# Performance work log

Measured on AMD Instinct MI355X. Metric: run time of the kernel, lower is better.

Reference implementation:

```python
import jax, jax.numpy as jnp
import numpy as np

NUM_BLOCKS = 16  # 4x4 grid of 2x2 blocks over the 8x8 matrix
E_BLK, H_BLK = 4, 2
E_CROSS, H_CROSS = 64, 8
VOCAB = 32000
LN_EPS = 1e-5


def _mha(x, Wqkv, bqkv, Wo, bo, nheads):
    """torch nn.MultiheadAttention (batch_first, self-attn, eval mode).
    Returns (out [B,T,E], attn weights averaged over heads [B,T,T])."""
    B, T, E = x.shape
    Dh = E // nheads
    qkv = x @ Wqkv.T + bqkv                      # [B,T,3E]
    q, k, v = jnp.split(qkv, 3, axis=-1)
    sp = lambda t: t.reshape(B, T, nheads, Dh).transpose(0, 2, 1, 3)  # [B,H,T,Dh]
    q, k, v = sp(q), sp(k), sp(v)
    scale = 1.0 / float(np.sqrt(Dh))
    scores = jnp.einsum('bhqd,bhkd->bhqk', q, k) * scale
    attn = jax.nn.softmax(scores, axis=-1)
    out = jnp.einsum('bhqk,bhkd->bhqd', attn, v).transpose(0, 2, 1, 3).reshape(B, T, E)
    return out @ Wo.T + bo, attn.mean(axis=1)


def _layernorm(x, g, b):
    mu = x.mean(-1, keepdims=True)
    var = x.var(-1, keepdims=True)
    return (x - mu) * jax.lax.rsqrt(var + LN_EPS) * g + b


def _to_blocks(M):
    # [B,T,8,8] -> [B,T,16,4]; block i = (row_blk*4+col_blk), 2x2 flattened row-major
    B, T = M.shape[:2]
    return jnp.transpose(M.reshape(B, T, 4, 2, 4, 2), (0, 1, 2, 4, 3, 5)).reshape(B, T, 16, 4)


def _from_blocks(x):
    # [B,T,16,4] -> [B,T,8,8]
    B, T = x.shape[:2]
    return jnp.transpose(x.reshape(B, T, 4, 4, 2, 2), (0, 1, 2, 4, 3, 5)).reshape(B, T, 8, 8)


def setup_inputs() -> dict:
    key = jax.random.key(0)
    ks = jax.random.split(key, 24)
    B, T = 4, 1024
    s = 0.05
    return {
        'M': jax.random.normal(ks[0], (B, T, 8, 8), jnp.float32),
        'token_ids': jax.random.randint(ks[1], (B, T), 0, VOCAB, jnp.int64),
        # 16 per-block MHA param sets (stacked)
        'Wqkv_blk': jax.random.normal(ks[2], (NUM_BLOCKS, 3 * E_BLK, E_BLK), jnp.float32) * s,
        'bqkv_blk': jnp.zeros((NUM_BLOCKS, 3 * E_BLK), jnp.float32),
        'Wo_blk': jax.random.normal(ks[3], (NUM_BLOCKS, E_BLK, E_BLK), jnp.float32) * s,
        'bo_blk': jnp.zeros((NUM_BLOCKS, E_BLK), jnp.float32),
        # cross-block MHA
        'Wqkv_c': jax.random.normal(ks[4], (3 * E_CROSS, E_CROSS), jnp.float32) * s,
        'bqkv_c': jnp.zeros((3 * E_CROSS,), jnp.float32),
        'Wo_c': jax.random.normal(ks[5], (E_CROSS, E_CROSS), jnp.float32) * s,
        'bo_c': jnp.zeros((E_CROSS,), jnp.float32),
        # FFN 64 -> 256 -> 64
        'W1': jax.random.normal(ks[6], (256, 64), jnp.float32) * s,
        'b1': jnp.zeros((256,), jnp.float32),
        'W2': jax.random.normal(ks[7], (64, 256), jnp.float32) * s,
        'b2': jnp.zeros((64,), jnp.float32),
        # LayerNorms
        'g1': jnp.ones((64,), jnp.float32), 'be1': jnp.zeros((64,), jnp.float32),
        'g2': jnp.ones((64,), jnp.float32), 'be2': jnp.zeros((64,), jnp.float32),
        # DynamicBlockSensitivity params
        'sens_emb': jax.random.normal(ks[8], (VOCAB, NUM_BLOCKS), jnp.float32) * s,
        'sens_alpha': jax.random.normal(ks[9], (NUM_BLOCKS,), jnp.float32) * s,
    }


def reference(M, token_ids, Wqkv_blk, bqkv_blk, Wo_blk, bo_blk,
              Wqkv_c, bqkv_c, Wo_c, bo_c, W1, b1, W2, b2,
              g1, be1, g2, be2, sens_emb, sens_alpha):
    B, T = M.shape[:2]
    blocks = _to_blocks(M)                                # [B,T,16,4]
    x_blk = jnp.moveaxis(blocks, 2, 0)                    # [16,B,T,4]
    blk_out, _ = jax.vmap(lambda x, W, b, Wo, bo: _mha(x, W, b, Wo, bo, H_BLK))(
        x_blk, Wqkv_blk, bqkv_blk, Wo_blk, bo_blk)        # [16,B,T,4]
    all_blocks = jnp.moveaxis(blk_out, 0, 2).reshape(B, T, 64)
    cross_out, attn_w = _mha(all_blocks, Wqkv_c, bqkv_c, Wo_c, bo_c, H_CROSS)
    all_blocks = _layernorm(all_blocks + cross_out, g1, be1)
    ffn = jax.nn.gelu(all_blocks @ W1.T + b1, approximate=False) @ W2.T + b2
    all_blocks = _layernorm(all_blocks + ffn, g2, be2)
    # Dynamic block sensitivity: token embedding + attention-received modulation
    attn_recv = attn_w.mean(axis=1)                       # [B,T] attention each token receives
    sens = jax.nn.sigmoid(sens_emb[token_ids] + attn_recv[..., None] * sens_alpha)  # [B,T,16]
    new_blocks = blocks + (all_blocks.reshape(B, T, 16, 4) - blocks) * sens[..., None]
    return _from_blocks(new_blocks)
```

## Files before the change

kernel.cpp:

```cpp
#include <hip/hip_runtime.h>
#include <hip/hip_bf16.h>
#include <math.h>

#define BB 4
#define TT 1024
#define BT 4096

#define OFF_BLOCKS 0
#define OFF_QKVB   262144
#define OFF_RECVP  262144
#define OFF_ALLB   1048576
#define OFF_QKVC   1310720
#define OFF_LC     2097152
#define OFF_ACCC   2129920
#define OFF_LN1    2396160
#define OFF_PARAMS 2658304
#define WS_FLOATS  2708624

#define P_W1T    0
#define P_W2T    16384
#define P_WQCT   32768
#define P_WOCT   45056
#define P_WOBLK  49152
#define P_BOBLK  49408
#define P_BQC    49472
#define P_BOC    49664
#define P_G1     49728
#define P_BE1    49792
#define P_B1     49856
#define P_B2     50112
#define P_G2     50176
#define P_BE2    50240
#define P_SAL    50304
#define P_TOTAL  50320

__device__ inline float rcpf(float x) { return __builtin_amdgcn_rcpf(x); }

typedef _Float16 h2 __attribute__((ext_vector_type(2)));
typedef __fp16   fh2 __attribute__((ext_vector_type(2)));

__device__ inline uint pkh(float a, float b) {
#if __has_builtin(__builtin_amdgcn_cvt_pkrtz)
  fh2 r = __builtin_amdgcn_cvt_pkrtz(a, b);
  return __builtin_bit_cast(uint, r);
#else
  h2 r = { (_Float16)a, (_Float16)b };
  return __builtin_bit_cast(uint, r);
#endif
}
__device__ inline h2 toh2(uint u) { return __builtin_bit_cast(h2, u); }

__device__ inline float dot2h(h2 a, h2 b, float c) {
#if __has_builtin(__builtin_amdgcn_fdot2)
  return __builtin_amdgcn_fdot2(a, b, c, false);
#else
  return c + (float)a.x * (float)b.x + (float)a.y * (float)b.y;
#endif
}

__device__ inline bool detect_bf16(const void* M) {
  const unsigned short* h = (const unsigned short*)M;
  unsigned short v = h[threadIdx.x & 63];
  int e = (v >> 7) & 0xff;
  unsigned long long m = __ballot((e >= 90) && (e <= 141));
  return __popcll(m) >= 58;
}

template <bool ISBF>
__device__ inline float ldf(const void* p, int i) {
  if (ISBF) return __bfloat162float(((const __hip_bfloat16*)p)[i]);
  else      return ((const float*)p)[i];
}

template <bool ISBF>
__global__ void __launch_bounds__(256) k_prep2(
    const void* __restrict__ M,
    const void* __restrict__ Wqkv_blk,
    const void* __restrict__ bqkv_blk,
    const void* __restrict__ W1, const void* __restrict__ W2,
    const void* __restrict__ Wqkv_c, const void* __restrict__ Wo_c,
    const void* __restrict__ Wo_blk, const void* __restrict__ bo_blk,
    const void* __restrict__ bqkv_c, const void* __restrict__ bo_c,
    const void* __restrict__ g1, const void* __restrict__ be1,
    const void* __restrict__ b1, const void* __restrict__ b2,
    const void* __restrict__ g2, const void* __restrict__ be2,
    const void* __restrict__ sens_al,
    float* __restrict__ blocks, float* __restrict__ qkv_blk,
    float* __restrict__ params) {
  if (detect_bf16(M) != ISBF) return;
  if (blockIdx.x < 256) {
    int g = blockIdx.x * 256 + threadIdx.x;
    int i = g >> 12, bt = g & 4095;
    int rb = i >> 2, cb = i & 3;
    float x[4];
    #pragma unroll
    for (int r = 0; r < 2; ++r)
      #pragma unroll
      for (int c = 0; c < 2; ++c)
        x[r*2+c] = ldf<ISBF>(M, bt*64 + (rb*2+r)*8 + cb*2 + c);
    float* bo = blocks + bt*64 + i*4;
    #pragma unroll
    for (int j = 0; j < 4; ++j) bo[j] = x[j];
    float* o = qkv_blk + (i*BT + bt) * 12;
    #pragma unroll
    for (int c = 0; c < 12; ++c) {
      float a = ldf<ISBF>(bqkv_blk, i*12 + c);
      #pragma unroll
      for (int j = 0; j < 4; ++j) a += ldf<ISBF>(Wqkv_blk, i*48 + c*4 + j) * x[j];
      o[c] = a;
    }
  } else {
    for (int o = (blockIdx.x - 256)*256 + threadIdx.x; o < P_TOTAL; o += 16*256) {
      float v;
      if      (o < 16384) { int j = o >> 8, h2_ = o & 255; v = ldf<ISBF>(W1, h2_*64 + j); }
      else if (o < 32768) { int q = o - 16384; int k = q >> 6, j = q & 63; v = ldf<ISBF>(W2, j*256 + k); }
      else if (o < 45056) { int q = o - 32768; int j = q / 192, c = q % 192; v = ldf<ISBF>(Wqkv_c, c*64 + j); }
      else if (o < 49152) { int q = o - 45056; int m = q >> 6, j = q & 63; v = ldf<ISBF>(Wo_c, j*64 + m); }
      else if (o < 49408) v = ldf<ISBF>(Wo_blk, o - 49152);
      else if (o < 49472) v = ldf<ISBF>(bo_blk, o - 49408);
      else if (o < 49664) v = ldf<ISBF>(bqkv_c, o - 49472);
      else if (o < 49728) v = ldf<ISBF>(bo_c,   o - 49664);
      else if (o < 49792) v = ldf<ISBF>(g1,     o - 49728);
      else if (o < 49856) v = ldf<ISBF>(be1,    o - 49792);
      else if (o < 50112) v = ldf<ISBF>(b1,     o - 49856);
      else if (o < 50176) v = ldf<ISBF>(b2,     o - 50112);
      else if (o < 50240) v = ldf<ISBF>(g2,     o - 50176);
      else if (o < 50304) v = ldf<ISBF>(be2,    o - 50240);
      else                v = ldf<ISBF>(sens_al, o - 50304);
      params[o] = v;
    }
  }
}

__global__ void __launch_bounds__(512) k_blk2(
    const float* __restrict__ qkv_blk,
    const float* __restrict__ params,
    float* __restrict__ all_blocks) {
  __shared__ __align__(16) uint lds[14464];
  float* qf  = (float*)lds;
  uint*  kvu = lds + 4096;
  float* red = (float*)(lds + 8192);
  int bid = blockIdx.x;
  int qt = bid & 7, b = (bid >> 3) & 3, i = bid >> 5;
  int tid = threadIdx.x;
  int wv = __builtin_amdgcn_readfirstlane(tid) >> 6;
  int ql = tid & 63;
  const float* slab = qkv_blk + (size_t)(i*BT + b*TT) * 12;
  #pragma unroll
  for (int rr = 0; rr < 2; ++rr) {
    int r = tid + rr*512;
    const float4* rp = (const float4*)(slab + (size_t)r*12);
    float4 x0 = rp[0], x1 = rp[1], x2 = rp[2];
    *(float4*)(qf + r*4) = x0;
    *(uint4*)(kvu + r*4) = make_uint4(pkh(x1.x,x1.y), pkh(x1.z,x1.w),
                                      pkh(x2.x,x2.y), pkh(x2.z,x2.w));
  }
  __syncthreads();
  int qa = qt*128 + ql, qb = qa + 64;
  const float S2 = 0.70710678f;
  float4 qav = *(const float4*)(qf + qa*4);
  float4 qbv = *(const float4*)(qf + qb*4);
  uint qa01 = pkh(qav.x*S2, qav.y*S2), qa23 = pkh(qav.z*S2, qav.w*S2);
  uint qb01 = pkh(qbv.x*S2, qbv.y*S2), qb23 = pkh(qbv.z*S2, qbv.w*S2);
  float la0=0.f, la1=0.f, aa00=0.f, aa01=0.f, aa10=0.f, aa11=0.f;
  float lb0=0.f, lb1=0.f, ab00=0.f, ab01=0.f, ab10=0.f, ab11=0.f;
  int kbeg = wv*128;
  #pragma unroll 4
  for (int k = kbeg; k < kbeg + 128; ++k) {
    uint4 kk = *(const uint4*)(kvu + k*4);
    h2 k01 = toh2(kk.x), k23 = toh2(kk.y);
    h2 v01 = toh2(kk.z), v23 = toh2(kk.w);
    float pa0 = __expf(dot2h(toh2(qa01), k01, 0.f));
    float pa1 = __expf(dot2h(toh2(qa23), k23, 0.f));
    float pb0 = __expf(dot2h(toh2(qb01), k01, 0.f));
    float pb1 = __expf(dot2h(toh2(qb23), k23, 0.f));
    la0 += pa0; aa00 += pa0*(float)v01.x; aa01 += pa0*(float)v01.y;
    la1 += pa1; aa10 += pa1*(float)v23.x; aa11 += pa1*(float)v23.y;
    lb0 += pb0; ab00 += pb0*(float)v01.x; ab01 += pb0*(float)v01.y;
    lb1 += pb1; ab10 += pb1*(float)v23.x; ab11 += pb1*(float)v23.y;
  }
  float* ra = red + ql*49 + wv*6;
  ra[0]=la0; ra[1]=la1; ra[2]=aa00; ra[3]=aa01; ra[4]=aa10; ra[5]=aa11;
  float* rb = red + (ql+64)*49 + wv*6;
  rb[0]=lb0; rb[1]=lb1; rb[2]=ab00; rb[3]=ab01; rb[4]=ab10; rb[5]=ab11;
  __syncthreads();
  if (tid < 128) {
    float s[6] = {0.f,0.f,0.f,0.f,0.f,0.f};
    #pragma unroll
    for (int w = 0; w < 8; ++w) {
      const float* p = red + tid*49 + w*6;
      #pragma unroll
      for (int c = 0; c < 6; ++c) s[c] += p[c];
    }
    float r0 = rcpf(s[0]), r1 = rcpf(s[1]);
    float o[4] = { s[2]*r0, s[3]*r0, s[4]*r1, s[5]*r1 };
    int q2 = qt*128 + tid;
    const float* pWo = params + P_WOBLK + i*16;
    float* outp = all_blocks + (size_t)(b*TT + q2)*64 + i*4;
    #pragma unroll
    for (int j = 0; j < 4; ++j) {
      float a = params[P_BOBLK + i*4 + j];
      #pragma unroll
      for (int m2 = 0; m2 < 4; ++m2) a += pWo[j*4 + m2] * o[m2];
      outp[j] = a;
    }
  }
}

__global__ void __launch_bounds__(256) k_qkv_c2(
    const float* __restrict__ all_blocks,
    const float* __restrict__ params,
    float* __restrict__ qkv_c) {
  __shared__ float w[12288];
  __shared__ float xs[256];
  int tid = threadIdx.x;
  int t0 = blockIdx.x * 4;
  {
    const float4* src = (const float4*)(params + P_WQCT);
    float4* dst = (float4*)w;
    #pragma unroll
    for (int i = tid; i < 3072; i += 256) dst[i] = src[i];
  }
  xs[tid] = all_blocks[t0*64 + tid];
  __syncthreads();
  int tt = tid >> 6, lane = tid & 63;
  int t = t0 + tt;
  const float* x = xs + tt*64;
  float a0 = params[P_BQC + lane];
  float a1 = params[P_BQC + 64 + lane];
  float a2 = params[P_BQC + 128 + lane];
  #pragma unroll 8
  for (int j = 0; j < 64; ++j) {
    const float* r = w + j*192;
    float xj = x[j];
    a0 += r[lane]       * xj;
    a1 += r[64 + lane]  * xj;
    a2 += r[128 + lane] * xj;
  }
  float* o = qkv_c + (size_t)t*192;
  o[lane] = a0; o[64 + lane] = a1; o[128 + lane] = a2;
}

__global__ void __launch_bounds__(1024) k_cross9(
    const float* __restrict__ qkv_c,
    float* __restrict__ acc_c,
    float* __restrict__ recv_part) {
  __shared__ __align__(16) uint lds[23680];
  uint*  Ku  = lds;
  uint*  Vu  = lds + 4096;
  float* red = (float*)(lds + 4096);
  uint*  qb_ = lds + 22656;
  int bid = blockIdx.x;
  int qt = bid & 7, h = (bid >> 3) & 7, b = bid >> 6;
  int tid = threadIdx.x;
  int wv = __builtin_amdgcn_readfirstlane(tid) >> 6;
  int ql = tid & 63;
  int h8 = h*8;
  const float* base = qkv_c + (size_t)b*TT*192;
  {
    int r = tid;
    const float4* kp = (const float4*)(base + (size_t)r*192 + 64 + h8);
    const float4* vp = (const float4*)(base + (size_t)r*192 + 128 + h8);
    float4 k0 = kp[0], k1 = kp[1], v0 = vp[0], v1 = vp[1];
    *(uint4*)(Ku + r*4) = make_uint4(pkh(k0.x,k0.y), pkh(k0.z,k0.w),
                                     pkh(k1.x,k1.y), pkh(k1.z,k1.w));
    *(uint4*)(Vu + r*4) = make_uint4(pkh(v0.x,v0.y), pkh(v0.z,v0.w),
                                     pkh(v1.x,v1.y), pkh(v1.z,v1.w));
  }
  int qa = qt*128 + ql, qbq = qa + 64;
  const float SC = 0.35355339f;
  uint qa01,qa23,qa45,qa67, qb01,qb23,qb45,qb67;
  {
    const float4* pa = (const float4*)(base + (size_t)qa*192 + h8);
    const float4* pb = (const float4*)(base + (size_t)qbq*192 + h8);
    float4 a0 = pa[0], a1 = pa[1], b0 = pb[0], b1 = pb[1];
    qa01 = pkh(a0.x*SC, a0.y*SC); qa23 = pkh(a0.z*SC, a0.w*SC);
    qa45 = pkh(a1.x*SC, a1.y*SC); qa67 = pkh(a1.z*SC, a1.w*SC);
    qb01 = pkh(b0.x*SC, b0.y*SC); qb23 = pkh(b0.z*SC, b0.w*SC);
    qb45 = pkh(b1.x*SC, b1.y*SC); qb67 = pkh(b1.z*SC, b1.w*SC);
  }
  __syncthreads();
  float la = 0.f, lb = 0.f, aca[8], acb[8];
  #pragma unroll
  for (int c = 0; c < 8; ++c) { aca[c] = 0.f; acb[c] = 0.f; }
  int kbeg = wv*64;
  #pragma unroll 4
  for (int k = kbeg; k < kbeg + 64; ++k) {
    uint4 kk = *(const uint4*)(Ku + k*4);
    uint4 vv = *(const uint4*)(Vu + k*4);
    h2 k01 = toh2(kk.x), k23 = toh2(kk.y), k45 = toh2(kk.z), k67 = toh2(kk.w);
    float sa = dot2h(toh2(qa01),k01, dot2h(toh2(qa23),k23,
               dot2h(toh2(qa45),k45, dot2h(toh2(qa67),k67, 0.f))));
    float sb = dot2h(toh2(qb01),k01, dot2h(toh2(qb23),k23,
               dot2h(toh2(qb45),k45, dot2h(toh2(qb67),k67, 0.f))));
    float pa = __expf(sa);
    float pb = __expf(sb);
    la += pa; lb += pb;
    h2 v01 = toh2(vv.x), v23 = toh2(vv.y), v45 = toh2(vv.z), v67 = toh2(vv.w);
    aca[0] += pa*(float)v01.x; aca[1] += pa*(float)v01.y;
    aca[2] += pa*(float)v23.x; aca[3] += pa*(float)v23.y;
    aca[4] += pa*(float)v45.x; aca[5] += pa*(float)v45.y;
    aca[6] += pa*(float)v67.x; aca[7] += pa*(float)v67.y;
    acb[0] += pb*(float)v01.x; acb[1] += pb*(float)v01.y;
    acb[2] += pb*(float)v23.x; acb[3] += pb*(float)v23.y;
    acb[4] += pb*(float)v45.x; acb[5] += pb*(float)v45.y;
    acb[6] += pb*(float)v67.x; acb[7] += pb*(float)v67.y;
  }
  __syncthreads();
  {
    float* ra = red + ql*145 + wv*9;
    ra[0] = la;
    #pragma unroll
    for (int c = 0; c < 8; ++c) ra[1+c] = aca[c];
    float* rb = red + (ql+64)*145 + wv*9;
    rb[0] = lb;
    #pragma unroll
    for (int c = 0; c < 8; ++c) rb[1+c] = acb[c];
    if (wv == 0) {
      *(uint4*)(qb_ + ql*8)      = make_uint4(qa01, qa23, qa45, qa67);
      *(uint4*)(qb_ + (ql+64)*8) = make_uint4(qb01, qb23, qb45, qb67);
    }
  }
  __syncthreads();
  if (tid < 128) {
    float ls = 0.f, as[8];
    #pragma unroll
    for (int c = 0; c < 8; ++c) as[c] = 0.f;
    #pragma unroll
    for (int w = 0; w < 16; ++w) {
      const float* p = red + tid*145 + w*9;
      ls += p[0];
      #pragma unroll
      for (int c = 0; c < 8; ++c) as[c] += p[1+c];
    }
    float invl = rcpf(ls);
    int q2 = qt*128 + tid;
    int idx = (b*8 + h)*TT + q2;
    float4 o0 = { as[0]*invl, as[1]*invl, as[2]*invl, as[3]*invl };
    float4 o1 = { as[4]*invl, as[5]*invl, as[6]*invl, as[7]*invl };
    float4* op = (float4*)(acc_c + (size_t)idx*8);
    op[0] = o0; op[1] = o1;
    ((float*)(qb_ + tid*8))[4] = -__log2f(ls);
  }
  __syncthreads();
  {
    int qh = wv >> 3, g = wv & 7;
    int p = g*64 + ql;
    uint4 ka = *(const uint4*)(Ku + p*4);
    uint4 kb = *(const uint4*)(Ku + (p+512)*4);
    h2 A0 = toh2(ka.x), A1 = toh2(ka.y), A2 = toh2(ka.z), A3 = toh2(ka.w);
    h2 B0 = toh2(kb.x), B1 = toh2(kb.y), B2 = toh2(kb.z), B3 = toh2(kb.w);
    float r0 = 0.f, r1 = 0.f;
    const uint* qrow = qb_ + qh*64*8;
    const float L2E = 1.44269504f;
    #pragma unroll 4
    for (int qq = 0; qq < 64; ++qq) {
      uint4 q4 = *(const uint4*)(qrow + qq*8);
      float mq = __uint_as_float(qrow[qq*8 + 4]);
      h2 Q0 = toh2(q4.x), Q1 = toh2(q4.y), Q2 = toh2(q4.z), Q3 = toh2(q4.w);
      float s0 = dot2h(Q0,A0, dot2h(Q1,A1, dot2h(Q2,A2, dot2h(Q3,A3, 0.f))));
      float s1 = dot2h(Q0,B0, dot2h(Q1,B1, dot2h(Q2,B2, dot2h(Q3,B3, 0.f))));
      r0 += exp2f(fmaf(s0, L2E, mq));
      r1 += exp2f(fmaf(s1, L2E, mq));
    }
    int src = h*16 + qt*2 + qh;
    recv_part[((size_t)(b*1024 + p      ))*128 + src] = r0;
    recv_part[((size_t)(b*1024 + p + 512))*128 + src] = r1;
  }
}

__global__ void __launch_bounds__(256) k_fin(
    const float* __restrict__ all_blocks,
    const float* __restrict__ acc_c,
    const float* __restrict__ params,
    float* __restrict__ ln1) {
  __shared__ float pvs[4*64];
  int tt = threadIdx.x >> 6, j = threadIdx.x & 63;
  int t = blockIdx.x*4 + tt;
  int b = t >> 10, tl = t & 1023;
  int h = j >> 3;
  int idx = (b*8 + h)*TT + tl;
  pvs[tt*64 + j] = acc_c[idx*8 + (j & 7)];
  __syncthreads();
  float a = params[P_BOC + j];
  const float* WoT = params + P_WOCT;
  const float* p = pvs + tt*64;
  #pragma unroll 8
  for (int m = 0; m < 64; ++m) a += WoT[m*64 + j] * p[m];
  float x = all_blocks[t*64 + j] + a;
  float s = x, s2 = x*x;
  #pragma unroll
  for (int off = 32; off; off >>= 1) { s += __shfl_xor(s, off); s2 += __shfl_xor(s2, off); }
  float mu  = s  * (1.f/64.f);
  float var = s2 * (1.f/64.f) - mu*mu;
  float y = (x - mu) * rsqrtf(var + 1e-5f) * params[P_G1 + j] + params[P_BE1 + j];
  ln1[t*64 + j] = y;
}

template <bool ISBF>
__global__ void __launch_bounds__(512) k_ffn_out2(
    const void* __restrict__ M,
    const float* __restrict__ ln1,
    const float* __restrict__ params,
    const float* __restrict__ blocks,
    const int* __restrict__ tok32,
    const float* __restrict__ recv_part,
    const void* __restrict__ sens_emb,
    void* __restrict__ out) {
  if (detect_bf16(M) != ISBF) return;
  __shared__ float w[16384];
  __shared__ float ld2[512];
  __shared__ float hbuf[2048];
  int tid = threadIdx.x;
  int t0 = blockIdx.x * 8;
  int wv = tid >> 6, lane = tid & 63;
  float recv;
  {
    int t = t0 + wv, b = t >> 10, k = t & 1023;
    const float* rp = recv_part + ((size_t)(b*1024 + k))*128;
    float s = rp[lane] + rp[lane + 64];
    #pragma unroll
    for (int off = 32; off; off >>= 1) s += __shfl_xor(s, off);
    recv = s * (1.f/8192.f);
  }
  ld2[lane*8 + wv] = ln1[(t0 + wv)*64 + lane];
  {
    const float4* src = (const float4*)(params + P_W1T);
    float4* dst = (float4*)w;
    #pragma unroll
    for (int i = tid; i < 4096; i += 512) dst[i] = src[i];
  }
  __syncthreads();
  {
    int g = tid >> 8, u = tid & 255;
    float a0, a1, a2, a3;
    a0 = a1 = a2 = a3 = params[P_B1 + u];
    #pragma unroll 8
    for (int j = 0; j < 64; ++j) {
      float wj = w[j*256 + u];
      float4 xj = *(const float4*)(ld2 + j*8 + g*4);
      a0 += wj*xj.x; a1 += wj*xj.y; a2 += wj*xj.z; a3 += wj*xj.w;
    }
    float av[4] = {a0, a1, a2, a3};
    #pragma unroll
    for (int t2 = 0; t2 < 4; ++t2) {
      float v = av[t2];
      float u2 = 1.5957691f*v + 0.07135481f*v*v*v;
      hbuf[(g*4 + t2)*256 + u] = v * rcpf(1.f + __expf(-u2));
    }
  }
  __syncthreads();
  {
    const float4* src = (const float4*)(params + P_W2T);
    float4* dst = (float4*)w;
    #pragma unroll
    for (int i = tid; i < 4096; i += 512) dst[i] = src[i];
  }
  __syncthreads();
  int j = lane;
  int t = t0 + wv, b = t >> 10;
  float y = params[P_B2 + j];
  const float* hb = hbuf + wv*256;
  #pragma unroll 8
  for (int k = 0; k < 256; ++k) y += w[k*64 + j] * hb[k];
  float z = ld2[j*8 + wv] + y;
  float s = z, s2 = z*z;
  #pragma unroll
  for (int off = 32; off; off >>= 1) { s += __shfl_xor(s, off); s2 += __shfl_xor(s2, off); }
  float mu  = s  * (1.f/64.f);
  float var = s2 * (1.f/64.f) - mu*mu;
  float y2 = (z - mu) * rsqrtf(var + 1e-5f) * params[P_G2 + j] + params[P_BE2 + j];
  bool is64 = ((tok32[1] | tok32[3] | tok32[5] | tok32[7]) == 0);
  int tok = is64 ? tok32[t*2] : tok32[t];
  int i = j >> 2, e = j & 3;
  float sv = ldf<ISBF>(sens_emb, tok*16 + i) + recv * params[P_SAL + i];
  float sg = rcpf(1.f + __expf(-sv));
  float blk = blocks[t*64 + j];
  float nb = blk + (y2 - blk) * sg;
  int rb = i >> 2, cb = i & 3, r = e >> 1, c = e & 1;
  int oidx = t*64 + (rb*2 + r)*8 + cb*2 + c;
  if (ISBF) ((__hip_bfloat16*)out)[oidx] = __float2bfloat16(nb);
  else      ((float*)out)[oidx] = nb;
}

extern "C" void kernel_launch(void* const* d_in, const int* in_sizes, int n_in,
                              void* d_out, int out_size, void* d_ws, size_t ws_size,
                              hipStream_t stream) {
  const void* M        = d_in[0];
  const int*  tok      = (const int*)d_in[1];
  const void* Wqkv_blk = d_in[2];
  const void* bqkv_blk = d_in[3];
  const void* Wo_blk   = d_in[4];
  const void* bo_blk   = d_in[5];
  const void* Wqkv_c   = d_in[6];
  const void* bqkv_c   = d_in[7];
  const void* Wo_c     = d_in[8];
  const void* bo_c     = d_in[9];
  const void* W1       = d_in[10];
  const void* b1       = d_in[11];
  const void* W2       = d_in[12];
  const void* b2       = d_in[13];
  const void* g1       = d_in[14];
  const void* be1      = d_in[15];
  const void* g2i      = d_in[16];
  const void* be2      = d_in[17];
  const void* sens_emb = d_in[18];
  const void* sens_al  = d_in[19];

  float* ws = (float*)d_ws;
  float* blocks    = ws + OFF_BLOCKS;
  float* qkv_blk   = ws + OFF_QKVB;
  float* recv_part = ws + OFF_RECVP;
  float* all_blk   = ws + OFF_ALLB;
  float* qkv_c     = ws + OFF_QKVC;
  float* acc_c     = ws + OFF_ACCC;
  float* ln1       = ws + OFF_LN1;
  float* params    = ws + OFF_PARAMS;

  k_prep2<true ><<<272, 256, 0, stream>>>(M, Wqkv_blk, bqkv_blk, W1, W2, Wqkv_c, Wo_c,
                                          Wo_blk, bo_blk, bqkv_c, bo_c, g1, be1, b1, b2,
                                          g2i, be2, sens_al, blocks, qkv_blk, params);
  k_prep2<false><<<272, 256, 0, stream>>>(M, Wqkv_blk, bqkv_blk, W1, W2, Wqkv_c, Wo_c,
                                          Wo_blk, bo_blk, bqkv_c, bo_c, g1, be1, b1, b2,
                                          g2i, be2, sens_al, blocks, qkv_blk, params);
  k_blk2<<<512, 512, 0, stream>>>(qkv_blk, params, all_blk);
  k_qkv_c2<<<1024, 256, 0, stream>>>(all_blk, params, qkv_c);
  k_cross9<<<256, 1024, 0, stream>>>(qkv_c, acc_c, recv_part);
  k_fin<<<1024, 256, 0, stream>>>(all_blk, acc_c, params, ln1);
  k_ffn_out2<true ><<<512, 512, 0, stream>>>(M, ln1, params, blocks, tok, recv_part,
                                             sens_emb, (void*)d_out);
  k_ffn_out2<false><<<512, 512, 0, stream>>>(M, ln1, params, blocks, tok, recv_part,
                                             sens_emb, (void*)d_out);
}
```

Baseline: 204.8 us.

## Merge dtype-dispatched launches, fold log2e into scales, restructure recv and FFN reductions

Replaces the paired bf16/fp32 template launches with single kernels that branch on detected dtype internally, removing two redundant launches. Folds log2(e) into the query scales so the attention loops use exp2f directly. Reorganises the cross-attention received-attention pass to combine partial sums in LDS, halving the recv_part width. Splits the FFN second matmul across waves with an LDS reduction so each wave covers a k-slice for all 8 tokens. Adds LDS traffic and extra barriers in exchange.

After: 217.8 us. 1.06x slower.

```diff
diff --git a/kernel.cpp b/kernel.cpp
--- a/kernel.cpp
+++ b/kernel.cpp
@@ -73,21 +73,13 @@
 }
 
 template <bool ISBF>
-__global__ void __launch_bounds__(256) k_prep2(
-    const void* __restrict__ M,
-    const void* __restrict__ Wqkv_blk,
-    const void* __restrict__ bqkv_blk,
-    const void* __restrict__ W1, const void* __restrict__ W2,
-    const void* __restrict__ Wqkv_c, const void* __restrict__ Wo_c,
-    const void* __restrict__ Wo_blk, const void* __restrict__ bo_blk,
-    const void* __restrict__ bqkv_c, const void* __restrict__ bo_c,
-    const void* __restrict__ g1, const void* __restrict__ be1,
-    const void* __restrict__ b1, const void* __restrict__ b2,
-    const void* __restrict__ g2, const void* __restrict__ be2,
-    const void* __restrict__ sens_al,
-    float* __restrict__ blocks, float* __restrict__ qkv_blk,
-    float* __restrict__ params) {
-  if (detect_bf16(M) != ISBF) return;
+__device__ void prep2_body(
+    const void* M, const void* Wqkv_blk, const void* bqkv_blk,
+    const void* W1, const void* W2, const void* Wqkv_c, const void* Wo_c,
+    const void* Wo_blk, const void* bo_blk, const void* bqkv_c, const void* bo_c,
+    const void* g1, const void* be1, const void* b1, const void* b2,
+    const void* g2, const void* be2, const void* sens_al,
+    float* blocks, float* qkv_blk, float* params) {
   if (blockIdx.x < 256) {
     int g = blockIdx.x * 256 + threadIdx.x;
     int i = g >> 12, bt = g & 4095;
@@ -130,6 +122,29 @@
       params[o] = v;
     }
   }
+}
+
+__global__ void __launch_bounds__(256) k_prep3(
+    const void* __restrict__ M, const void* __restrict__ Wqkv_blk,
+    const void* __restrict__ bqkv_blk,
+    const void* __restrict__ W1, const void* __restrict__ W2,
+    const void* __restrict__ Wqkv_c, const void* __restrict__ Wo_c,
+    const void* __restrict__ Wo_blk, const void* __restrict__ bo_blk,
+    const void* __restrict__ bqkv_c, const void* __restrict__ bo_c,
+    const void* __restrict__ g1, const void* __restrict__ be1,
+    const void* __restrict__ b1, const void* __restrict__ b2,
+    const void* __restrict__ g2, const void* __restrict__ be2,
+    const void* __restrict__ sens_al,
+    float* __restrict__ blocks, float* __restrict__ qkv_blk,
+    float* __restrict__ params) {
+  if (detect_bf16(M))
+    prep2_body<true >(M, Wqkv_blk, bqkv_blk, W1, W2, Wqkv_c, Wo_c, Wo_blk, bo_blk,
+                      bqkv_c, bo_c, g1, be1, b1, b2, g2, be2, sens_al,
+                      blocks, qkv_blk, params);
+  else
+    prep2_body<false>(M, Wqkv_blk, bqkv_blk, W1, W2, Wqkv_c, Wo_c, Wo_blk, bo_blk,
+                      bqkv_c, bo_c, g1, be1, b1, b2, g2, be2, sens_al,
+                      blocks, qkv_blk, params);
 }
 
 __global__ void __launch_bounds__(512) k_blk2(
@@ -157,11 +172,11 @@
   }
   __syncthreads();
   int qa = qt*128 + ql, qb = qa + 64;
-  const float S2 = 0.70710678f;
+  const float S2L = 0.70710678f * 1.44269504f;
   float4 qav = *(const float4*)(qf + qa*4);
   float4 qbv = *(const float4*)(qf + qb*4);
-  uint qa01 = pkh(qav.x*S2, qav.y*S2), qa23 = pkh(qav.z*S2, qav.w*S2);
-  uint qb01 = pkh(qbv.x*S2, qbv.y*S2), qb23 = pkh(qbv.z*S2, qbv.w*S2);
+  uint qa01 = pkh(qav.x*S2L, qav.y*S2L), qa23 = pkh(qav.z*S2L, qav.w*S2L);
+  uint qb01 = pkh(qbv.x*S2L, qbv.y*S2L), qb23 = pkh(qbv.z*S2L, qbv.w*S2L);
   float la0=0.f, la1=0.f, aa00=0.f, aa01=0.f, aa10=0.f, aa11=0.f;
   float lb0=0.f, lb1=0.f, ab00=0.f, ab01=0.f, ab10=0.f, ab11=0.f;
   int kbeg = wv*128;
@@ -170,10 +185,10 @@
     uint4 kk = *(const uint4*)(kvu + k*4);
     h2 k01 = toh2(kk.x), k23 = toh2(kk.y);
     h2 v01 = toh2(kk.z), v23 = toh2(kk.w);
-    float pa0 = __expf(dot2h(toh2(qa01), k01, 0.f));
-    float pa1 = __expf(dot2h(toh2(qa23), k23, 0.f));
-    float pb0 = __expf(dot2h(toh2(qb01), k01, 0.f));
-    float pb1 = __expf(dot2h(toh2(qb23), k23, 0.f));
+    float pa0 = exp2f(dot2h(toh2(qa01), k01, 0.f));
+    float pa1 = exp2f(dot2h(toh2(qa23), k23, 0.f));
+    float pb0 = exp2f(dot2h(toh2(qb01), k01, 0.f));
+    float pb1 = exp2f(dot2h(toh2(qb23), k23, 0.f));
     la0 += pa0; aa00 += pa0*(float)v01.x; aa01 += pa0*(float)v01.y;
     la1 += pa1; aa10 += pa1*(float)v23.x; aa11 += pa1*(float)v23.y;
     lb0 += pb0; ab00 += pb0*(float)v01.x; ab01 += pb0*(float)v01.y;
@@ -241,15 +256,16 @@
   o[lane] = a0; o[64 + lane] = a1; o[128 + lane] = a2;
 }
 
-__global__ void __launch_bounds__(1024) k_cross9(
+__global__ void __launch_bounds__(1024) k_cross10(
     const float* __restrict__ qkv_c,
     float* __restrict__ acc_c,
     float* __restrict__ recv_part) {
   __shared__ __align__(16) uint lds[23680];
-  uint*  Ku  = lds;
-  uint*  Vu  = lds + 4096;
-  float* red = (float*)(lds + 4096);
-  uint*  qb_ = lds + 22656;
+  uint*  Ku   = lds;
+  uint*  Vu   = lds + 4096;
+  float* red  = (float*)(lds + 4096);
+  float* rcmb = (float*)(lds + 4096);
+  uint*  qb_  = lds + 22656;
   int bid = blockIdx.x;
   int qt = bid & 7, h = (bid >> 3) & 7, b = bid >> 6;
   int tid = threadIdx.x;
@@ -268,16 +284,16 @@
                                      pkh(v1.x,v1.y), pkh(v1.z,v1.w));
   }
   int qa = qt*128 + ql, qbq = qa + 64;
-  const float SC = 0.35355339f;
+  const float SCL = 0.35355339f * 1.44269504f;
   uint qa01,qa23,qa45,qa67, qb01,qb23,qb45,qb67;
   {
     const float4* pa = (const float4*)(base + (size_t)qa*192 + h8);
     const float4* pb = (const float4*)(base + (size_t)qbq*192 + h8);
     float4 a0 = pa[0], a1 = pa[1], b0 = pb[0], b1 = pb[1];
-    qa01 = pkh(a0.x*SC, a0.y*SC); qa23 = pkh(a0.z*SC, a0.w*SC);
-    qa45 = pkh(a1.x*SC, a1.y*SC); qa67 = pkh(a1.z*SC, a1.w*SC);
-    qb01 = pkh(b0.x*SC, b0.y*SC); qb23 = pkh(b0.z*SC, b0.w*SC);
-    qb45 = pkh(b1.x*SC, b1.y*SC); qb67 = pkh(b1.z*SC, b1.w*SC);
+    qa01 = pkh(a0.x*SCL, a0.y*SCL); qa23 = pkh(a0.z*SCL, a0.w*SCL);
+    qa45 = pkh(a1.x*SCL, a1.y*SCL); qa67 = pkh(a1.z*SCL, a1.w*SCL);
+    qb01 = pkh(b0.x*SCL, b0.y*SCL); qb23 = pkh(b0.z*SCL, b0.w*SCL);
+    qb45 = pkh(b1.x*SCL, b1.y*SCL); qb67 = pkh(b1.z*SCL, b1.w*SCL);
   }
   __syncthreads();
   float la = 0.f, lb = 0.f, aca[8], acb[8];
@@ -289,12 +305,12 @@
     uint4 kk = *(const uint4*)(Ku + k*4);
     uint4 vv = *(const uint4*)(Vu + k*4);
     h2 k01 = toh2(kk.x), k23 = toh2(kk.y), k45 = toh2(kk.z), k67 = toh2(kk.w);
-    float sa = dot2h(toh2(qa01),k01, dot2h(toh2(qa23),k23,
-               dot2h(toh2(qa45),k45, dot2h(toh2(qa67),k67, 0.f))));
-    float sb = dot2h(toh2(qb01),k01, dot2h(toh2(qb23),k23,
-               dot2h(toh2(qb45),k45, dot2h(toh2(qb67),k67, 0.f))));
-    float pa = __expf(sa);
-    float pb = __expf(sb);
+    float sa = dot2h(toh2(qa01),k01, dot2h(toh2(qa23),k23, 0.f))
+             + dot2h(toh2(qa45),k45, dot2h(toh2(qa67),k67, 0.f));
+    float sb = dot2h(toh2(qb01),k01, dot2h(toh2(qb23),k23, 0.f))
+             + dot2h(toh2(qb45),k45, dot2h(toh2(qb67),k67, 0.f));
+    float pa = exp2f(sa);
+    float pb = exp2f(sb);
     la += pa; lb += pb;
     h2 v01 = toh2(vv.x), v23 = toh2(vv.y), v45 = toh2(vv.z), v67 = toh2(vv.w);
     aca[0] += pa*(float)v01.x; aca[1] += pa*(float)v01.y;
@@ -344,28 +360,43 @@
   }
   __syncthreads();
   {
-    int qh = wv >> 3, g = wv & 7;
+    int qq = wv >> 2, g = wv & 3;
     int p = g*64 + ql;
     uint4 ka = *(const uint4*)(Ku + p*4);
-    uint4 kb = *(const uint4*)(Ku + (p+512)*4);
-    h2 A0 = toh2(ka.x), A1 = toh2(ka.y), A2 = toh2(ka.z), A3 = toh2(ka.w);
-    h2 B0 = toh2(kb.x), B1 = toh2(kb.y), B2 = toh2(kb.z), B3 = toh2(kb.w);
-    float r0 = 0.f, r1 = 0.f;
-    const uint* qrow = qb_ + qh*64*8;
-    const float L2E = 1.44269504f;
+    uint4 kb = *(const uint4*)(Ku + (p+256)*4);
+    uint4 kc = *(const uint4*)(Ku + (p+512)*4);
+    uint4 kd = *(const uint4*)(Ku + (p+768)*4);
+    float r0 = 0.f, r1 = 0.f, r2 = 0.f, r3 = 0.f;
+    const uint* qrow = qb_ + qq*32*8;
     #pragma unroll 4
-    for (int qq = 0; qq < 64; ++qq) {
-      uint4 q4 = *(const uint4*)(qrow + qq*8);
-      float mq = __uint_as_float(qrow[qq*8 + 4]);
+    for (int q = 0; q < 32; ++q) {
+      uint4 q4 = *(const uint4*)(qrow + q*8);
+      float mq = __uint_as_float(qrow[q*8 + 4]);
       h2 Q0 = toh2(q4.x), Q1 = toh2(q4.y), Q2 = toh2(q4.z), Q3 = toh2(q4.w);
-      float s0 = dot2h(Q0,A0, dot2h(Q1,A1, dot2h(Q2,A2, dot2h(Q3,A3, 0.f))));
-      float s1 = dot2h(Q0,B0, dot2h(Q1,B1, dot2h(Q2,B2, dot2h(Q3,B3, 0.f))));
-      r0 += exp2f(fmaf(s0, L2E, mq));
-      r1 += exp2f(fmaf(s1, L2E, mq));
-    }
-    int src = h*16 + qt*2 + qh;
-    recv_part[((size_t)(b*1024 + p      ))*128 + src] = r0;
-    recv_part[((size_t)(b*1024 + p + 512))*128 + src] = r1;
+      float s0 = dot2h(Q0,toh2(ka.x), dot2h(Q1,toh2(ka.y), 0.f))
+               + dot2h(Q2,toh2(ka.z), dot2h(Q3,toh2(ka.w), 0.f));
+      float s1 = dot2h(Q0,toh2(kb.x), dot2h(Q1,toh2(kb.y), 0.f))
+               + dot2h(Q2,toh2(kb.z), dot2h(Q3,toh2(kb.w), 0.f));
+      float s2 = dot2h(Q0,toh2(kc.x), dot2h(Q1,toh2(kc.y), 0.f))
+               + dot2h(Q2,toh2(kc.z), dot2h(Q3,toh2(kc.w), 0.f));
+      float s3 = dot2h(Q0,toh2(kd.x), dot2h(Q1,toh2(kd.y), 0.f))
+               + dot2h(Q2,toh2(kd.z), dot2h(Q3,toh2(kd.w), 0.f));
+      r0 += exp2f(s0 + mq);
+      r1 += exp2f(s1 + mq);
+      r2 += exp2f(s2 + mq);
+      r3 += exp2f(s3 + mq);
+    }
+    rcmb[(p      )*4 + qq] = r0;
+    rcmb[(p + 256)*4 + qq] = r1;
+    rcmb[(p + 512)*4 + qq] = r2;
+    rcmb[(p + 768)*4 + qq] = r3;
+  }
+  __syncthreads();
+  {
+    int k = tid;
+    float4 v = *(const float4*)(rcmb + k*4);
+    int src = h*8 + qt;
+    recv_part[((size_t)(b*1024 + k))*64 + src] = v.x + v.y + v.z + v.w;
   }
 }
 
@@ -398,7 +429,104 @@
 }
 
 template <bool ISBF>
-__global__ void __launch_bounds__(512) k_ffn_out2(
+__device__ void ffn_body(
+    const float* ln1, const float* params, const float* blocks,
+    const int* tok32, const float* recv_part, const void* sens_emb, void* out,
+    float* w, float* ld2, float* hbuf) {
+  int tid = threadIdx.x;
+  int t0 = blockIdx.x * 8;
+  int wv = tid >> 6, lane = tid & 63;
+  float recv;
+  {
+    int t = t0 + wv, b = t >> 10, k = t & 1023;
+    const float* rp = recv_part + ((size_t)(b*1024 + k))*64;
+    float s = rp[lane];
+    #pragma unroll
+    for (int off = 32; off; off >>= 1) s += __shfl_xor(s, off);
+    recv = s * (1.f/8192.f);
+  }
+  ld2[lane*8 + wv] = ln1[(t0 + wv)*64 + lane];
+  {
+    const float4* src = (const float4*)(params + P_W1T);
+    float4* dst = (float4*)w;
+    #pragma unroll
+    for (int i = tid; i < 4096; i += 512) dst[i] = src[i];
+  }
+  __syncthreads();
+  {
+    int g = tid >> 8, u = tid & 255;
+    float a0, a1, a2, a3;
+    a0 = a1 = a2 = a3 = params[P_B1 + u];
+    #pragma unroll 8
+    for (int j = 0; j < 64; ++j) {
+      float wj = w[j*256 + u];
+      float4 xj = *(const float4*)(ld2 + j*8 + g*4);
+      a0 += wj*xj.x; a1 += wj*xj.y; a2 += wj*xj.z; a3 += wj*xj.w;
+    }
+    float av[4] = {a0, a1, a2, a3};
+    float4 hv;
+    #pragma unroll
+    for (int t2 = 0; t2 < 4; ++t2) {
+      float v = av[t2];
+      float u2 = 1.5957691f*v + 0.07135481f*v*v*v;
+      ((float*)&hv)[t2] = v * rcpf(1.f + __expf(-u2));
+    }
+    *(float4*)(hbuf + u*8 + g*4) = hv;
+  }
+  __syncthreads();
+  {
+    const float4* src = (const float4*)(params + P_W2T);
+    float4* dst = (float4*)w;
+    #pragma unroll
+    for (int i = tid; i < 4096; i += 512) dst[i] = src[i];
+  }
+  __syncthreads();
+  float yp[8] = {0.f,0.f,0.f,0.f,0.f,0.f,0.f,0.f};
+  {
+    int j = lane, k0 = wv*32;
+    #pragma unroll 8
+    for (int k = k0; k < k0 + 32; ++k) {
+      float wkj = w[k*64 + j];
+      float4 h03 = *(const float4*)(hbuf + k*8);
+      float4 h47 = *(const float4*)(hbuf + k*8 + 4);
+      yp[0] += wkj*h03.x; yp[1] += wkj*h03.y; yp[2] += wkj*h03.z; yp[3] += wkj*h03.w;
+      yp[4] += wkj*h47.x; yp[5] += wkj*h47.y; yp[6] += wkj*h47.z; yp[7] += wkj*h47.w;
+    }
+  }
+  __syncthreads();
+  float* red2 = w;
+  {
+    #pragma unroll
+    for (int t2 = 0; t2 < 8; ++t2) red2[wv*520 + t2*64 + lane] = yp[t2];
+  }
+  __syncthreads();
+  int j = lane;
+  int tok = wv;
+  int t = t0 + tok, b = t >> 10;
+  float y = params[P_B2 + j];
+  #pragma unroll
+  for (int wq = 0; wq < 8; ++wq) y += red2[wq*520 + tok*64 + j];
+  float z = ld2[j*8 + tok] + y;
+  float s = z, s2 = z*z;
+  #pragma unroll
+  for (int off = 32; off; off >>= 1) { s += __shfl_xor(s, off); s2 += __shfl_xor(s2, off); }
+  float mu  = s  * (1.f/64.f);
+  float var = s2 * (1.f/64.f) - mu*mu;
+  float y2 = (z - mu) * rsqrtf(var + 1e-5f) * params[P_G2 + j] + params[P_BE2 + j];
+  bool is64 = ((tok32[1] | tok32[3] | tok32[5] | tok32[7]) == 0);
+  int tk = is64 ? tok32[t*2] : tok32[t];
+  int i = j >> 2, e = j & 3;
+  float sv = ldf<ISBF>(sens_emb, tk*16 + i) + recv * params[P_SAL + i];
+  float sg = rcpf(1.f + __expf(-sv));
+  float blk = blocks[t*64 + j];
+  float nb = blk + (y2 - blk) * sg;
+  int rb = i >> 2, cb = i & 3, r = e >> 1, c = e & 1;
+  int oidx = t*64 + (rb*2 + r)*8 + cb*2 + c;
+  if (ISBF) ((__hip_bfloat16*)out)[oidx] = __float2bfloat16(nb);
+  else      ((float*)out)[oidx] = nb;
+}
+
+__global__ void __launch_bounds__(512) k_ffn_out3(
     const void* __restrict__ M,
     const float* __restrict__ ln1,
     const float* __restrict__ params,
@@ -407,80 +535,13 @@
     const float* __restrict__ recv_part,
     const void* __restrict__ sens_emb,
     void* __restrict__ out) {
-  if (detect_bf16(M) != ISBF) return;
   __shared__ float w[16384];
   __shared__ float ld2[512];
   __shared__ float hbuf[2048];
-  int tid = threadIdx.x;
-  int t0 = blockIdx.x * 8;
-  int wv = tid >> 6, lane = tid & 63;
-  float recv;
-  {
-    int t = t0 + wv, b = t >> 10, k = t & 1023;
-    const float* rp = recv_part + ((size_t)(b*1024 + k))*128;
-    float s = rp[lane] + rp[lane + 64];
-    #pragma unroll
-    for (int off = 32; off; off >>= 1) s += __shfl_xor(s, off);
-    recv = s * (1.f/8192.f);
-  }
-  ld2[lane*8 + wv] = ln1[(t0 + wv)*64 + lane];
-  {
-    const float4* src = (const float4*)(params + P_W1T);
-    float4* dst = (float4*)w;
-    #pragma unroll
-    for (int i = tid; i < 4096; i += 512) dst[i] = src[i];
-  }
-  __syncthreads();
-  {
-    int g = tid >> 8, u = tid & 255;
-    float a0, a1, a2, a3;
-    a0 = a1 = a2 = a3 = params[P_B1 + u];
-    #pragma unroll 8
-    for (int j = 0; j < 64; ++j) {
-      float wj = w[j*256 + u];
-      float4 xj = *(const float4*)(ld2 + j*8 + g*4);
-      a0 += wj*xj.x; a1 += wj*xj.y; a2 += wj*xj.z; a3 += wj*xj.w;
-    }
-    float av[4] = {a0, a1, a2, a3};
-    #pragma unroll
-    for (int t2 = 0; t2 < 4; ++t2) {
-      float v = av[t2];
-      float u2 = 1.5957691f*v + 0.07135481f*v*v*v;
-      hbuf[(g*4 + t2)*256 + u] = v * rcpf(1.f + __expf(-u2));
-    }
-  }
-  __syncthreads();
-  {
-    const float4* src = (const float4*)(params + P_W2T);
-    float4* dst = (float4*)w;
-    #pragma unroll
-    for (int i = tid; i < 4096; i += 512) dst[i] = src[i];
-  }
-  __syncthreads();
-  int j = lane;
-  int t = t0 + wv, b = t >> 10;
-  float y = params[P_B2 + j];
-  const float* hb = hbuf + wv*256;
-  #pragma unroll 8
-  for (int k = 0; k < 256; ++k) y += w[k*64 + j] * hb[k];
-  float z = ld2[j*8 + wv] + y;
-  float s = z, s2 = z*z;
-  #pragma unroll
-  for (int off = 32; off; off >>= 1) { s += __shfl_xor(s, off); s2 += __shfl_xor(s2, off); }
-  float mu  = s  * (1.f/64.f);
-  float var = s2 * (1.f/64.f) - mu*mu;
-  float y2 = (z - mu) * rsqrtf(var + 1e-5f) * params[P_G2 + j] + params[P_BE2 + j];
-  bool is64 = ((tok32[1] | tok32[3] | tok32[5] | tok32[7]) == 0);
-  int tok = is64 ? tok32[t*2] : tok32[t];
-  int i = j >> 2, e = j & 3;
-  float sv = ldf<ISBF>(sens_emb, tok*16 + i) + recv * params[P_SAL + i];
-  float sg = rcpf(1.f + __expf(-sv));
-  float blk = blocks[t*64 + j];
-  float nb = blk + (y2 - blk) * sg;
-  int rb = i >> 2, cb = i & 3, r = e >> 1, c = e & 1;
-  int oidx = t*64 + (rb*2 + r)*8 + cb*2 + c;
-  if (ISBF) ((__hip_bfloat16*)out)[oidx] = __float2bfloat16(nb);
-  else      ((float*)out)[oidx] = nb;
+  if (detect_bf16(M))
+    ffn_body<true >(ln1, params, blocks, tok32, recv_part, sens_emb, out, w, ld2, hbuf);
+  else
+    ffn_body<false>(ln1, params, blocks, tok32, recv_part, sens_emb, out, w, ld2, hbuf);
 }
 
 extern "C" void kernel_launch(void* const* d_in, const int* in_sizes, int n_in,
@@ -517,18 +578,13 @@
   float* ln1       = ws + OFF_LN1;
   float* params    = ws + OFF_PARAMS;
 
-  k_prep2<true ><<<272, 256, 0, stream>>>(M, Wqkv_blk, bqkv_blk, W1, W2, Wqkv_c, Wo_c,
-                                          Wo_blk, bo_blk, bqkv_c, bo_c, g1, be1, b1, b2,
-                                          g2i, be2, sens_al, blocks, qkv_blk, params);
-  k_prep2<false><<<272, 256, 0, stream>>>(M, Wqkv_blk, bqkv_blk, W1, W2, Wqkv_c, Wo_c,
-                                          Wo_blk, bo_blk, bqkv_c, bo_c, g1, be1, b1, b2,
-                                          g2i, be2, sens_al, blocks, qkv_blk, params);
+  k_prep3<<<272, 256, 0, stream>>>(M, Wqkv_blk, bqkv_blk, W1, W2, Wqkv_c, Wo_c,
+                                   Wo_blk, bo_blk, bqkv_c, bo_c, g1, be1, b1, b2,
+                                   g2i, be2, sens_al, blocks, qkv_blk, params);
   k_blk2<<<512, 512, 0, stream>>>(qkv_blk, params, all_blk);
   k_qkv_c2<<<1024, 256, 0, stream>>>(all_blk, params, qkv_c);
-  k_cross9<<<256, 1024, 0, stream>>>(qkv_c, acc_c, recv_part);
+  k_cross10<<<256, 1024, 0, stream>>>(qkv_c, acc_c, recv_part);
   k_fin<<<1024, 256, 0, stream>>>(all_blk, acc_c, params, ln1);
-  k_ffn_out2<true ><<<512, 512, 0, stream>>>(M, ln1, params, blocks, tok, recv_part,
-                                             sens_emb, (void*)d_out);
-  k_ffn_out2<false><<<512, 512, 0, stream>>>(M, ln1, params, blocks, tok, recv_part,
-                                             sens_emb, (void*)d_out);
-}
+  k_ffn_out3<<<512, 512, 0, stream>>>(M, ln1, params, blocks, tok, recv_part,
+                                      sens_emb, (void*)d_out);
+}
```
